# Optimization experiments

Hardware: AMD Instinct MI355X
Metric: run time of the kernel (lower is better)

Reference implementation:

```python
import jax, jax.numpy as jnp
import numpy as np

N, D, S, E, EL, ITERS = 250_000, 128, 6, 500_000, 50_000, 4


def setup_inputs() -> dict:
    key = jax.random.key(0)
    ks = jax.random.split(key, 16)
    s = 1.0 / np.sqrt(D)  # keep activations O(1)
    return {
        'feat':   jax.random.normal(ks[0], (N, D), jnp.float32),
        'pre_u':  jax.random.randint(ks[1], (S, E), 0, N, jnp.int32),
        'pre_v':  jax.random.randint(ks[2], (S, E), 0, N, jnp.int32),
        'suc_u':  jax.random.randint(ks[3], (S, E), 0, N, jnp.int32),
        'suc_v':  jax.random.randint(ks[4], (S, E), 0, N, jnp.int32),
        'left_u': jax.random.randint(ks[5], (EL,), 0, N, jnp.int32),
        'left_v': jax.random.randint(ks[6], (EL,), 0, N, jnp.int32),
        'right_u': jax.random.randint(ks[7], (EL,), 0, N, jnp.int32),
        'right_v': jax.random.randint(ks[8], (EL,), 0, N, jnp.int32),
        'W_ctr':   jax.random.normal(ks[9],  (ITERS, D, D), jnp.float32) * s,
        'W_pre':   jax.random.normal(ks[10], (ITERS, S, D, D), jnp.float32) * s,
        'W_suc':   jax.random.normal(ks[11], (ITERS, S, D, D), jnp.float32) * s,
        'W_left':  jax.random.normal(ks[12], (ITERS, D, D), jnp.float32) * s,
        'W_right': jax.random.normal(ks[13], (ITERS, D, D), jnp.float32) * s,
        'gn1_w': jnp.ones((ITERS, D), jnp.float32),
        'gn1_b': jnp.zeros((ITERS, D), jnp.float32),
        'W_ctr2':  jax.random.normal(ks[14], (ITERS, D, D), jnp.float32) * s,
        'gn2_w': jnp.ones((ITERS, D), jnp.float32),
        'gn2_b': jnp.zeros((ITERS, D), jnp.float32),
    }


def _gn(x, w, b, eps=1e-5):
    # torch GroupNorm(1, D) on a [N, D] input: per-row normalization over channels
    mu = jnp.mean(x, -1, keepdims=True)
    var = jnp.mean((x - mu) ** 2, -1, keepdims=True)
    return (x - mu) * jax.lax.rsqrt(var + eps) * w + b


def reference(feat, pre_u, pre_v, suc_u, suc_v, left_u, left_v, right_u, right_v,
              W_ctr, W_pre, W_suc, W_left, W_right, gn1_w, gn1_b,
              W_ctr2, gn2_w, gn2_b):
    res = feat
    for i in range(ITERS):  # 4 fusion iterations, structurally distinct weights
        temp = feat @ W_ctr[i].T  # nn.Linear(bias=False): x @ W.T
        for k in range(S):  # 6 dilation scales, pre and suc edges
            temp = temp.at[pre_u[k]].add(feat[pre_v[k]] @ W_pre[i, k].T)
            temp = temp.at[suc_u[k]].add(feat[suc_v[k]] @ W_suc[i, k].T)
        temp = temp.at[left_u].add(feat[left_v] @ W_left[i].T)
        temp = temp.at[right_u].add(feat[right_v] @ W_right[i].T)
        h = jax.nn.relu(_gn(temp, gn1_w[i], gn1_b[i]))           # fuse['norm'] + relu
        h = _gn(h @ W_ctr2[i].T, gn2_w[i], gn2_b[i])             # fuse['ctr2']: Linear+GN, no act
        feat = jax.nn.relu(h + res)                              # residual + relu
        res = feat
    return feat
```

## Files before the change

kernel.cpp:

```cpp
#include <hip/hip_runtime.h>


#define NN 250000
#define DD 128
#define EE 500000
#define ELE 50000
#define NITER 4
#define NL 14
#define M14 (NL*NN)
#define TOTE (12*EE + 2*ELE)
#define KBIG (15*DD)
#define BK 64
#define TILES_TOTAL ((NN + 127)/128)
#define NBKT TILES_TOTAL
#define BCAP 4096
#define LK (128*NL)
#define NBLK_BUCKET 256
#define EPB ((TOTE + NBLK_BUCKET - 1)/NBLK_BUCKET)

typedef unsigned short u16;
typedef __attribute__((ext_vector_type(4))) float f32x4;
typedef __attribute__((ext_vector_type(8))) __bf16 bf16x8;

static __device__ __forceinline__ unsigned f2bf(float f) {
  unsigned u = __float_as_uint(f);
  return (u + 0x7fffu + ((u >> 16) & 1u)) >> 16;
}
static __device__ __forceinline__ float bflo(unsigned w){ return __uint_as_float(w << 16); }
static __device__ __forceinline__ float bfhi(unsigned w){ return __uint_as_float(w & 0xffff0000u); }

static __device__ __forceinline__ void gload16(const u16* g, u16* l) {
  __builtin_amdgcn_global_load_lds(
      (const __attribute__((address_space(1))) void*)g,
      (__attribute__((address_space(3))) void*)l, 16, 0, 0);
}

static __device__ __forceinline__ int edge_u(int idx,
    const int* __restrict__ pu, const int* __restrict__ su,
    const int* __restrict__ lu, const int* __restrict__ ru) {
  if (idx < 12*EE) {
    int l = idx / EE; int e = idx - l*EE;
    return (l < 6) ? pu[l*EE + e] : su[(l-6)*EE + e];
  }
  int r = idx - 12*EE;
  return (r < ELE) ? lu[r] : ru[r - ELE];
}

static __device__ __forceinline__ void edge_luv(int idx,
    const int* __restrict__ pu, const int* __restrict__ pv,
    const int* __restrict__ su, const int* __restrict__ sv,
    const int* __restrict__ lu, const int* __restrict__ lv,
    const int* __restrict__ ru, const int* __restrict__ rv,
    int& l, int& u, int& v) {
  if (idx < 12*EE) {
    l = idx / EE; int e = idx - l*EE;
    if (l < 6) { u = pu[l*EE+e]; v = pv[l*EE+e]; }
    else       { u = su[(l-6)*EE+e]; v = sv[(l-6)*EE+e]; }
  } else {
    int r = idx - 12*EE;
    if (r < ELE) { l = 12; u = lu[r]; v = lv[r]; }
    else         { l = 13; u = ru[r-ELE]; v = rv[r-ELE]; }
  }
}

__global__ __launch_bounds__(1024) void k_bucket(
    const int* __restrict__ pu, const int* __restrict__ pv,
    const int* __restrict__ su, const int* __restrict__ sv,
    const int* __restrict__ lu, const int* __restrict__ lv,
    const int* __restrict__ ru, const int* __restrict__ rv,
    int* __restrict__ bcur, unsigned* __restrict__ bstage) {
  __shared__ int cnt[NBKT];
  __shared__ int cur[NBKT];
  int t = threadIdx.x;
  for (int i=t; i<NBKT; i+=1024) cnt[i] = 0;
  __syncthreads();
  int e0 = blockIdx.x * EPB;
  int e1 = e0 + EPB; if (e1 > TOTE) e1 = TOTE;
  for (int idx = e0 + t; idx < e1; idx += 1024) {
    int u = edge_u(idx, pu, su, lu, ru);
    atomicAdd(&cnt[u >> 7], 1);
  }
  __syncthreads();
  for (int i=t; i<NBKT; i+=1024) {
    int c = cnt[i];
    cur[i] = c ? atomicAdd(&bcur[i], c) : 0;
  }
  __syncthreads();
  for (int idx = e0 + t; idx < e1; idx += 1024) {
    int l, u, v;
    edge_luv(idx, pu, pv, su, sv, lu, lv, ru, rv, l, u, v);
    int b = u >> 7;
    unsigned rec = ((unsigned)((u & 127)*NL + l) << 18) | (unsigned)v;
    int pos = atomicAdd(&cur[b], 1);
    if (pos < BCAP) bstage[(size_t)b*BCAP + pos] = rec;
  }
}

__global__ void k_bscan(const int* __restrict__ bcur, int* __restrict__ bbase,
                        int* __restrict__ rowptr) {
  __shared__ int wsum[4];
  int t = threadIdx.x, lane = t & 63, w = t >> 6;
  int v[8]; int s = 0;
  #pragma unroll
  for (int j=0;j<8;j++){
    int idx = t*8 + j;
    int x = 0;
    if (idx < NBKT) { x = bcur[idx]; if (x > BCAP) x = BCAP; }
    v[j] = s; s += x;
  }
  int ps = s;
  for (int d=1; d<64; d<<=1) { int o = __shfl_up(ps, d); if (lane >= d) ps += o; }
  if (lane == 63) wsum[w] = ps;
  __syncthreads();
  int woff = 0;
  for (int j=0;j<w;j++) woff += wsum[j];
  int excl = woff + ps - s;
  #pragma unroll
  for (int j=0;j<8;j++){
    int idx = t*8 + j;
    if (idx < NBKT) bbase[idx] = excl + v[j];
  }
  if (t == 255) rowptr[M14] = excl + s;
}

__global__ __launch_bounds__(256) void k_place(const unsigned* __restrict__ bstage,
    const int* __restrict__ bcur, const int* __restrict__ bbase,
    int* __restrict__ rowptr, int* __restrict__ edge_v) {
  __shared__ int lh[LK];
  __shared__ int lex[LK];
  __shared__ int wsum[4];
  int b = blockIdx.x, t = threadIdx.x;
  int lane = t & 63, w = t >> 6;
  int cnt = bcur[b]; if (cnt > BCAP) cnt = BCAP;
  int base = bbase[b];
  const unsigned* rec = bstage + (size_t)b*BCAP;
  for (int i=t; i<LK; i+=256) lh[i] = 0;
  __syncthreads();
  for (int e=t; e<cnt; e+=256) atomicAdd(&lh[rec[e]>>18], 1);
  __syncthreads();
  int s = 0;
  int my[7];
  #pragma unroll
  for (int j=0;j<7;j++){ my[j] = s; s += lh[t*7+j]; }
  int ps = s;
  for (int d=1; d<64; d<<=1) { int o = __shfl_up(ps, d); if (lane >= d) ps += o; }
  if (lane == 63) wsum[w] = ps;
  __syncthreads();
  int woff = 0;
  for (int j=0;j<w;j++) woff += wsum[j];
  int excl = woff + ps - s;
  #pragma unroll
  for (int j=0;j<7;j++) lex[t*7+j] = excl + my[j];
  __syncthreads();
  for (int i=t; i<LK; i+=256) rowptr[(size_t)b*LK + i] = base + lex[i];
  for (int i=t; i<LK; i+=256) lh[i] = lex[i];
  __syncthreads();
  for (int e=t; e<cnt; e+=256) {
    unsigned r = rec[e];
    int pos = atomicAdd(&lh[r>>18], 1);
    edge_v[base + pos] = (int)(r & 0x3FFFFu);
  }
}

__global__ void k_f2bf(const float* __restrict__ in, unsigned* __restrict__ out) {
  int i = blockIdx.x*256 + threadIdx.x;
  float2 v = ((const float2*)in)[i];
  out[i] = f2bf(v.x) | (f2bf(v.y) << 16);
}

__global__ void k_bw(const float* __restrict__ Wc, const float* __restrict__ Wp,
                     const float* __restrict__ Ws, const float* __restrict__ Wl,
                     const float* __restrict__ Wr, const float* __restrict__ Wc2,
                     int it, u16* __restrict__ wcat, u16* __restrict__ wc2) {
  int i = blockIdx.x*256 + threadIdx.x;
  if (i < 128*KBIG) {
    int r = i / KBIG, K = i - r*KBIG;
    int s = K >> 7, c = K & 127;
    float val;
    if (s == 0)       val = Wc[(it*128 + r)*128 + c];
    else if (s <= 6)  val = Wp[((it*6 + (s-1))*128 + r)*128 + c];
    else if (s <= 12) val = Ws[((it*6 + (s-7))*128 + r)*128 + c];
    else if (s == 13) val = Wl[(it*128 + r)*128 + c];
    else              val = Wr[(it*128 + r)*128 + c];
    wcat[i] = (u16)f2bf(val);
  } else {
    int j = i - 128*KBIG;
    wc2[j] = (u16)f2bf(Wc2[it*16384 + j]);
  }
}

__global__ __launch_bounds__(256) void k_agg(const unsigned* __restrict__ featbf,
    const int* __restrict__ rowptr, const int* __restrict__ edge_v,
    unsigned* __restrict__ X, int chunk_base) {
  int wid = threadIdx.x >> 6, lane = threadIdx.x & 63;
  int nl = blockIdx.x*4 + wid;
  int node = chunk_base + nl;
  size_t xb = (size_t)nl * (14*64);
  if (node >= NN) {
    #pragma unroll
    for (int s=0;s<14;s++) X[xb + s*64 + lane] = 0;
    return;
  }
  int rp = 0;
  if (lane < 15) rp = rowptr[node*NL + lane];
  int st0 = __shfl(rp, 0);
  int cnt = __shfl(rp, 14) - st0;
  float ax = 0.f, ay = 0.f;
  int s = 0;
  int nextb = __shfl(rp, 1);
  int vv = 0;
  for (int base = 0; base < cnt; base += 8) {
    if ((base & 63) == 0) vv = edge_v[st0 + base + lane];
    unsigned wrow[8];
    int m = cnt - base; if (m > 8) m = 8;
    #pragma unroll
    for (int q=0;q<8;q++)
      if (q < m) {
        int v = __shfl(vv, (base & 63) + q);
        wrow[q] = featbf[(size_t)v*64 + lane];
      }
    for (int q=0;q<m;q++) {
      int e = st0 + base + q;
      while (e == nextb && s < 14) {
        X[xb + s*64 + lane] = f2bf(ax) | (f2bf(ay) << 16);
        ax = 0.f; ay = 0.f; s++;
        int ni = s + 1; if (ni > 14) ni = 14;
        nextb = __shfl(rp, ni);
      }
      ax += bflo(wrow[q]); ay += bfhi(wrow[q]);
    }
  }
  while (s < 14) {
    X[xb + s*64 + lane] = f2bf(ax) | (f2bf(ay) << 16);
    ax = 0.f; ay = 0.f; s++;
  }
}

__global__ __launch_bounds__(256) void gemm_big(
    const u16* __restrict__ Xc, const u16* __restrict__ fbf,
    const u16* __restrict__ B, unsigned* __restrict__ hbf,
    const float* __restrict__ gw, const float* __restrict__ gb, int row0_abs) {
  __shared__ u16 smem[2*128*BK];
  u16* As = smem; u16* Bs = smem + 128*BK;
  int tid = threadIdx.x, wid = tid >> 6, lane = tid & 63;
  int wm = wid >> 1, wn = wid & 1;
  int tile_row = blockIdx.x * 128;
  f32x4 acc[4][4] = {};
  int srow = lane >> 3, scol = (lane & 7) * 8;
  for (int k0 = 0; k0 < KBIG; k0 += BK) {
    __syncthreads();
    if (k0 < DD) {
      #pragma unroll
      for (int j=0;j<4;j++) {
        int seg = wid + j*4; int r = seg*8 + srow;
        int arow = row0_abs + tile_row + r; if (arow > NN-1) arow = NN-1;
        gload16(fbf + (size_t)arow*DD + (k0 + scol), &As[seg*512]);
        gload16(B + (size_t)r*KBIG + (k0 + scol), &Bs[seg*512]);
      }
    } else {
      #pragma unroll
      for (int j=0;j<4;j++) {
        int seg = wid + j*4; int r = seg*8 + srow;
        gload16(Xc + (size_t)(tile_row + r)*(14*128) + (k0 - DD + scol), &As[seg*512]);
        gload16(B + (size_t)r*KBIG + (k0 + scol), &Bs[seg*512]);
      }
    }
    __syncthreads();
    #pragma unroll
    for (int kk=0; kk<2; kk++) {
      bf16x8 af[4], bfr[4];
      #pragma unroll
      for (int mt=0; mt<4; mt++)
        af[mt] = *(const bf16x8*)&As[(wm*64 + mt*16 + (lane&15))*BK + kk*32 + ((lane>>4)*8)];
      #pragma unroll
      for (int nt=0; nt<4; nt++)
        bfr[nt] = *(const bf16x8*)&Bs[(wn*64 + nt*16 + (lane&15))*BK + kk*32 + ((lane>>4)*8)];
      #pragma unroll
      for (int mt=0; mt<4; mt++)
        #pragma unroll
        for (int nt=0; nt<4; nt++)
          acc[mt][nt] = __builtin_amdgcn_mfma_f32_16x16x32_bf16(af[mt], bfr[nt], acc[mt][nt], 0, 0, 0);
    }
  }
  float* Cs = (float*)smem;
  float2 wv = ((const float2*)gw)[lane];
  float2 bv = ((const float2*)gb)[lane];
  #pragma unroll
  for (int ph=0; ph<2; ph++) {
    __syncthreads();
    if (wm == ph) {
      #pragma unroll
      for (int mt=0;mt<4;mt++)
        #pragma unroll
        for (int nt=0;nt<4;nt++)
          #pragma unroll
          for (int r=0;r<4;r++)
            Cs[(size_t)(mt*16 + ((lane>>4)<<2) + r)*128 + wn*64 + nt*16 + (lane&15)] = acc[mt][nt][r];
    }
    __syncthreads();
    for (int rr=0; rr<16; rr++) {
      int lrow = wid*16 + rr;
      int grow = row0_abs + tile_row + ph*64 + lrow;
      float2 x = ((float2*)(Cs + lrow*128))[lane];
      float s = x.x + x.y, sq = x.x*x.x + x.y*x.y;
      #pragma unroll
      for (int d=1; d<64; d<<=1) { s += __shfl_xor(s,d); sq += __shfl_xor(sq,d); }
      float mu = s*(1.f/DD), var = sq*(1.f/DD) - mu*mu;
      float rs = rsqrtf(var + 1e-5f);
      if (grow < NN) {
        float y0 = fmaxf(fmaf((x.x-mu)*rs, wv.x, bv.x), 0.f);
        float y1 = fmaxf(fmaf((x.y-mu)*rs, wv.y, bv.y), 0.f);
        hbf[(size_t)grow*64 + lane] = f2bf(y0) | (f2bf(y1) << 16);
      }
    }
  }
}

__global__ __launch_bounds__(256) void gemm_sm(
    const u16* __restrict__ A, const u16* __restrict__ B,
    const float* __restrict__ res, float* __restrict__ out32,
    unsigned* __restrict__ featbf,
    const float* __restrict__ gw, const float* __restrict__ gb) {
  __shared__ u16 smem[2*128*BK];
  u16* As = smem; u16* Bs = smem + 128*BK;
  int tid = threadIdx.x, wid = tid >> 6, lane = tid & 63;
  int wm = wid >> 1, wn = wid & 1;
  int tile_row = blockIdx.x * 128;
  f32x4 acc[4][4] = {};
  int srow = lane >> 3, scol = (lane & 7) * 8;
  for (int k0 = 0; k0 < DD; k0 += BK) {
    __syncthreads();
    #pragma unroll
    for (int j=0;j<4;j++) {
      int seg = wid + j*4; int r = seg*8 + srow;
      gload16(A + (size_t)(tile_row + r)*DD + (k0 + scol), &As[seg*512]);
      gload16(B + (size_t)r*DD + (k0 + scol), &Bs[seg*512]);
    }
    __syncthreads();
    #pragma unroll
    for (int kk=0; kk<2; kk++) {
      bf16x8 af[4], bfr[4];
      #pragma unroll
      for (int mt=0; mt<4; mt++)
        af[mt] = *(const bf16x8*)&As[(wm*64 + mt*16 + (lane&15))*BK + kk*32 + ((lane>>4)*8)];
      #pragma unroll
      for (int nt=0; nt<4; nt++)
        bfr[nt] = *(const bf16x8*)&Bs[(wn*64 + nt*16 + (lane&15))*BK + kk*32 + ((lane>>4)*8)];
      #pragma unroll
      for (int mt=0; mt<4; mt++)
        #pragma unroll
        for (int nt=0; nt<4; nt++)
          acc[mt][nt] = __builtin_amdgcn_mfma_f32_16x16x32_bf16(af[mt], bfr[nt], acc[mt][nt], 0, 0, 0);
    }
  }
  float* Cs = (float*)smem;
  float2 wv = ((const float2*)gw)[lane];
  float2 bv = ((const float2*)gb)[lane];
  #pragma unroll
  for (int ph=0; ph<2; ph++) {
    __syncthreads();
    if (wm == ph) {
      #pragma unroll
      for (int mt=0;mt<4;mt++)
        #pragma unroll
        for (int nt=0;nt<4;nt++)
          #pragma unroll
          for (int r=0;r<4;r++)
            Cs[(size_t)(mt*16 + ((lane>>4)<<2) + r)*128 + wn*64 + nt*16 + (lane&15)] = acc[mt][nt][r];
    }
    __syncthreads();
    for (int rr=0; rr<16; rr++) {
      int lrow = wid*16 + rr;
      int grow = tile_row + ph*64 + lrow;
      float2 x = ((float2*)(Cs + lrow*128))[lane];
      float s = x.x + x.y, sq = x.x*x.x + x.y*x.y;
      #pragma unroll
      for (int d=1; d<64; d<<=1) { s += __shfl_xor(s,d); sq += __shfl_xor(sq,d); }
      float mu = s*(1.f/DD), var = sq*(1.f/DD) - mu*mu;
      float rs = rsqrtf(var + 1e-5f);
      if (grow < NN) {
        float2 rv = ((const float2*)(res + (size_t)grow*DD))[lane];
        float o0 = fmaxf(fmaf((x.x-mu)*rs, wv.x, bv.x) + rv.x, 0.f);
        float o1 = fmaxf(fmaf((x.y-mu)*rs, wv.y, bv.y) + rv.y, 0.f);
        ((float2*)(out32 + (size_t)grow*DD))[lane] = make_float2(o0, o1);
        featbf[(size_t)grow*64 + lane] = f2bf(o0) | (f2bf(o1) << 16);
      }
    }
  }
}

extern "C" void kernel_launch(void* const* d_in, const int* in_sizes, int n_in,
                              void* d_out, int out_size, void* d_ws, size_t ws_size,
                              hipStream_t stream) {
  const float* feat_in = (const float*)d_in[0];
  const int* pre_u  = (const int*)d_in[1];
  const int* pre_v  = (const int*)d_in[2];
  const int* suc_u  = (const int*)d_in[3];
  const int* suc_v  = (const int*)d_in[4];
  const int* left_u = (const int*)d_in[5];
  const int* left_v = (const int*)d_in[6];
  const int* right_u= (const int*)d_in[7];
  const int* right_v= (const int*)d_in[8];
  const float* W_ctr  = (const float*)d_in[9];
  const float* W_pre  = (const float*)d_in[10];
  const float* W_suc  = (const float*)d_in[11];
  const float* W_left = (const float*)d_in[12];
  const float* W_right= (const float*)d_in[13];
  const float* gn1w   = (const float*)d_in[14];
  const float* gn1b   = (const float*)d_in[15];
  const float* W_ctr2 = (const float*)d_in[16];
  const float* gn2w   = (const float*)d_in[17];
  const float* gn2b   = (const float*)d_in[18];

  char* ws = (char*)d_ws;
  size_t off = 0;
  auto alloc = [&](size_t bytes) -> char* {
    char* p = ws + off; off += (bytes + 255) & ~(size_t)255; return p;
  };
  float*    feat32 = (float*)   alloc((size_t)NN*DD*4);
  unsigned* featbf = (unsigned*)alloc((size_t)NN*64*4);
  unsigned* hbf    = (unsigned*)alloc((size_t)TILES_TOTAL*128*64*4);
  u16*      wcat   = (u16*)     alloc((size_t)128*KBIG*2);
  u16*      wc2    = (u16*)     alloc((size_t)128*128*2);
  int*      rowptr = (int*)     alloc(((size_t)NBKT*LK + 1)*4);
  int*      edge_v = (int*)     alloc((size_t)(TOTE + 64)*4);
  unsigned* bstage = (unsigned*)alloc((size_t)NBKT*BCAP*4);
  int*      bcur   = (int*)     alloc((size_t)NBKT*4);
  int*      bbase  = (int*)     alloc((size_t)NBKT*4);

  size_t tile_bytes = (size_t)128*(14*128)*2;
  size_t avail = (ws_size > off + 65536) ? (ws_size - off - 65536) : 0;
  int chunk_tiles = (int)(avail / tile_bytes);
  if (chunk_tiles > 256) chunk_tiles = 256;
  if (chunk_tiles < 8) chunk_tiles = 8;
  unsigned* Xc = (unsigned*)alloc((size_t)chunk_tiles * tile_bytes);
  int nchunk = (TILES_TOTAL + chunk_tiles - 1) / chunk_tiles;
  (void)in_sizes; (void)n_in; (void)out_size;

  hipMemsetAsync(bcur, 0, (size_t)NBKT*4, stream);
  k_bucket<<<NBLK_BUCKET, 1024, 0, stream>>>(pre_u, pre_v, suc_u, suc_v,
                                             left_u, left_v, right_u, right_v,
                                             bcur, bstage);
  k_bscan<<<1, 256, 0, stream>>>(bcur, bbase, rowptr);
  k_place<<<NBKT, 256, 0, stream>>>(bstage, bcur, bbase, rowptr, edge_v);

  k_f2bf<<<NN*64/256, 256, 0, stream>>>(feat_in, featbf);

  for (int it = 0; it < NITER; it++) {
    k_bw<<<1024, 256, 0, stream>>>(W_ctr, W_pre, W_suc, W_left, W_right, W_ctr2, it, wcat, wc2);
    for (int c = 0; c < nchunk; c++) {
      int tile0 = c*chunk_tiles;
      int tiles = (TILES_TOTAL - tile0 < chunk_tiles) ? (TILES_TOTAL - tile0) : chunk_tiles;
      int base  = tile0*128;
      k_agg<<<tiles*32, 256, 0, stream>>>(featbf, rowptr, edge_v, Xc, base);
      gemm_big<<<tiles, 256, 0, stream>>>((const u16*)Xc, (const u16*)featbf, wcat,
                                          hbf, gn1w + it*DD, gn1b + it*DD, base);
    }
    gemm_sm<<<TILES_TOTAL, 256, 0, stream>>>((const u16*)hbf, wc2,
        (it == 0 ? feat_in : feat32),
        (it == NITER-1 ? (float*)d_out : feat32), featbf,
        gn2w + it*DD, gn2b + it*DD);
  }
}
```

Measured before the change: 4.939 ms.

## Fuse ctr2 GEMM and second GroupNorm into the aggregation GEMM epilogue

The separate second-GEMM kernel is merged into the main GEMM: the GN1+ReLU output is kept as bf16 in shared memory and multiplied by W_ctr2 in the same block. GN2, the residual add and the ReLU then run directly on MFMA accumulator registers, with per-row statistics reduced through shuffles and a small shared array. This removes the hbf intermediate and the fp32 feature round trip. The residual now comes from ping-pong bf16 feature buffers, which loses some precision compared with the fp32 residual. Shared-memory tiles also get an XOR swizzle to reduce bank conflicts.

```diff
diff --git a/kernel.cpp b/kernel.cpp
--- a/kernel.cpp
+++ b/kernel.cpp
@@ -236,33 +236,39 @@
   }
 }
 
-__global__ __launch_bounds__(256) void gemm_big(
+__global__ __launch_bounds__(256) void gemm_fused(
     const u16* __restrict__ Xc, const u16* __restrict__ fbf,
-    const u16* __restrict__ B, unsigned* __restrict__ hbf,
-    const float* __restrict__ gw, const float* __restrict__ gb, int row0_abs) {
+    const u16* __restrict__ Bw, const u16* __restrict__ wc2g,
+    unsigned* __restrict__ fout, float* __restrict__ out32, int last,
+    const float* __restrict__ g1w, const float* __restrict__ g1b,
+    const float* __restrict__ g2w, const float* __restrict__ g2b,
+    int row0_abs) {
   __shared__ u16 smem[2*128*BK];
+  __shared__ float stats[2][128][2];
   u16* As = smem; u16* Bs = smem + 128*BK;
   int tid = threadIdx.x, wid = tid >> 6, lane = tid & 63;
   int wm = wid >> 1, wn = wid & 1;
+  int g = lane >> 4, l15 = lane & 15, l7 = lane & 7;
   int tile_row = blockIdx.x * 128;
   f32x4 acc[4][4] = {};
-  int srow = lane >> 3, scol = (lane & 7) * 8;
+  int srow8 = lane >> 3;
+  int scol = ((lane & 7) ^ srow8) * 8;
   for (int k0 = 0; k0 < KBIG; k0 += BK) {
     __syncthreads();
     if (k0 < DD) {
       #pragma unroll
       for (int j=0;j<4;j++) {
-        int seg = wid + j*4; int r = seg*8 + srow;
+        int seg = wid + j*4; int r = seg*8 + srow8;
         int arow = row0_abs + tile_row + r; if (arow > NN-1) arow = NN-1;
         gload16(fbf + (size_t)arow*DD + (k0 + scol), &As[seg*512]);
-        gload16(B + (size_t)r*KBIG + (k0 + scol), &Bs[seg*512]);
+        gload16(Bw + (size_t)r*KBIG + (k0 + scol), &Bs[seg*512]);
       }
     } else {
       #pragma unroll
       for (int j=0;j<4;j++) {
-        int seg = wid + j*4; int r = seg*8 + srow;
+        int seg = wid + j*4; int r = seg*8 + srow8;
         gload16(Xc + (size_t)(tile_row + r)*(14*128) + (k0 - DD + scol), &As[seg*512]);
-        gload16(B + (size_t)r*KBIG + (k0 + scol), &Bs[seg*512]);
+        gload16(Bw + (size_t)r*KBIG + (k0 + scol), &Bs[seg*512]);
       }
     }
     __syncthreads();
@@ -271,10 +277,10 @@
       bf16x8 af[4], bfr[4];
       #pragma unroll
       for (int mt=0; mt<4; mt++)
-        af[mt] = *(const bf16x8*)&As[(wm*64 + mt*16 + (lane&15))*BK + kk*32 + ((lane>>4)*8)];
+        af[mt] = *(const bf16x8*)&As[((wm*64 + mt*16 + l15)*BK + kk*32 + g*8) ^ (l7<<3)];
       #pragma unroll
       for (int nt=0; nt<4; nt++)
-        bfr[nt] = *(const bf16x8*)&Bs[(wn*64 + nt*16 + (lane&15))*BK + kk*32 + ((lane>>4)*8)];
+        bfr[nt] = *(const bf16x8*)&Bs[((wn*64 + nt*16 + l15)*BK + kk*32 + g*8) ^ (l7<<3)];
       #pragma unroll
       for (int mt=0; mt<4; mt++)
         #pragma unroll
@@ -282,111 +288,112 @@
           acc[mt][nt] = __builtin_amdgcn_mfma_f32_16x16x32_bf16(af[mt], bfr[nt], acc[mt][nt], 0, 0, 0);
     }
   }
-  float* Cs = (float*)smem;
-  float2 wv = ((const float2*)gw)[lane];
-  float2 bv = ((const float2*)gb)[lane];
-  #pragma unroll
-  for (int ph=0; ph<2; ph++) {
-    __syncthreads();
-    if (wm == ph) {
-      #pragma unroll
-      for (int mt=0;mt<4;mt++)
-        #pragma unroll
-        for (int nt=0;nt<4;nt++)
-          #pragma unroll
-          for (int r=0;r<4;r++)
-            Cs[(size_t)(mt*16 + ((lane>>4)<<2) + r)*128 + wn*64 + nt*16 + (lane&15)] = acc[mt][nt][r];
-    }
-    __syncthreads();
-    for (int rr=0; rr<16; rr++) {
-      int lrow = wid*16 + rr;
-      int grow = row0_abs + tile_row + ph*64 + lrow;
-      float2 x = ((float2*)(Cs + lrow*128))[lane];
-      float s = x.x + x.y, sq = x.x*x.x + x.y*x.y;
-      #pragma unroll
-      for (int d=1; d<64; d<<=1) { s += __shfl_xor(s,d); sq += __shfl_xor(sq,d); }
-      float mu = s*(1.f/DD), var = sq*(1.f/DD) - mu*mu;
+  __syncthreads();
+
+  #pragma unroll
+  for (int mt=0; mt<4; mt++)
+    #pragma unroll
+    for (int r=0; r<4; r++) {
+      float s = 0.f, q = 0.f;
+      #pragma unroll
+      for (int nt=0; nt<4; nt++) { float v = acc[mt][nt][r]; s += v; q += v*v; }
+      #pragma unroll
+      for (int d=1; d<16; d<<=1) { s += __shfl_xor(s, d); q += __shfl_xor(q, d); }
+      if (l15 == 0) {
+        int R = wm*64 + mt*16 + g*4 + r;
+        stats[wn][R][0] = s; stats[wn][R][1] = q;
+      }
+    }
+  __syncthreads();
+
+  float w1[4], b1[4], w2[4], b2[4];
+  #pragma unroll
+  for (int nt=0; nt<4; nt++) {
+    int C = wn*64 + nt*16 + l15;
+    w1[nt] = g1w[C]; b1[nt] = g1b[C];
+    w2[nt] = g2w[C]; b2[nt] = g2b[C];
+  }
+  #pragma unroll
+  for (int mt=0; mt<4; mt++)
+    #pragma unroll
+    for (int r=0; r<4; r++) {
+      int R = wm*64 + mt*16 + g*4 + r;
+      float ts = stats[0][R][0] + stats[1][R][0];
+      float tq = stats[0][R][1] + stats[1][R][1];
+      float mu = ts*(1.f/DD), var = tq*(1.f/DD) - mu*mu;
       float rs = rsqrtf(var + 1e-5f);
-      if (grow < NN) {
-        float y0 = fmaxf(fmaf((x.x-mu)*rs, wv.x, bv.x), 0.f);
-        float y1 = fmaxf(fmaf((x.y-mu)*rs, wv.y, bv.y), 0.f);
-        hbf[(size_t)grow*64 + lane] = f2bf(y0) | (f2bf(y1) << 16);
-      }
-    }
-  }
-}
-
-__global__ __launch_bounds__(256) void gemm_sm(
-    const u16* __restrict__ A, const u16* __restrict__ B,
-    const float* __restrict__ res, float* __restrict__ out32,
-    unsigned* __restrict__ featbf,
-    const float* __restrict__ gw, const float* __restrict__ gb) {
-  __shared__ u16 smem[2*128*BK];
-  u16* As = smem; u16* Bs = smem + 128*BK;
-  int tid = threadIdx.x, wid = tid >> 6, lane = tid & 63;
-  int wm = wid >> 1, wn = wid & 1;
-  int tile_row = blockIdx.x * 128;
-  f32x4 acc[4][4] = {};
-  int srow = lane >> 3, scol = (lane & 7) * 8;
-  for (int k0 = 0; k0 < DD; k0 += BK) {
-    __syncthreads();
-    #pragma unroll
-    for (int j=0;j<4;j++) {
-      int seg = wid + j*4; int r = seg*8 + srow;
-      gload16(A + (size_t)(tile_row + r)*DD + (k0 + scol), &As[seg*512]);
-      gload16(B + (size_t)r*DD + (k0 + scol), &Bs[seg*512]);
-    }
-    __syncthreads();
-    #pragma unroll
-    for (int kk=0; kk<2; kk++) {
-      bf16x8 af[4], bfr[4];
-      #pragma unroll
-      for (int mt=0; mt<4; mt++)
-        af[mt] = *(const bf16x8*)&As[(wm*64 + mt*16 + (lane&15))*BK + kk*32 + ((lane>>4)*8)];
+      #pragma unroll
+      for (int nt=0; nt<4; nt++) {
+        int C = wn*64 + nt*16 + l15;
+        float y = fmaxf(fmaf((acc[mt][nt][r]-mu)*rs, w1[nt], b1[nt]), 0.f);
+        float p = __shfl_xor(y, 1);
+        if (!(lane & 1)) {
+          unsigned word = f2bf(y) | (f2bf(p) << 16);
+          int idx = (R*128 + (C & ~1)) ^ ((R&7)<<3);
+          *(unsigned*)&smem[idx] = word;
+        }
+      }
+    }
+  __syncthreads();
+
+  f32x4 a2[4][4] = {};
+  #pragma unroll
+  for (int kk2=0; kk2<4; kk2++) {
+    bf16x8 wf[4], hf[4];
+    #pragma unroll
+    for (int nt=0; nt<4; nt++)
+      wf[nt] = *(const bf16x8*)&wc2g[(size_t)(wn*64 + nt*16 + l15)*DD + kk2*32 + g*8];
+    #pragma unroll
+    for (int mt=0; mt<4; mt++)
+      hf[mt] = *(const bf16x8*)&smem[((wm*64 + mt*16 + l15)*DD + kk2*32 + g*8) ^ (l7<<3)];
+    #pragma unroll
+    for (int mt=0; mt<4; mt++)
       #pragma unroll
       for (int nt=0; nt<4; nt++)
-        bfr[nt] = *(const bf16x8*)&Bs[(wn*64 + nt*16 + (lane&15))*BK + kk*32 + ((lane>>4)*8)];
-      #pragma unroll
-      for (int mt=0; mt<4; mt++)
-        #pragma unroll
-        for (int nt=0; nt<4; nt++)
-          acc[mt][nt] = __builtin_amdgcn_mfma_f32_16x16x32_bf16(af[mt], bfr[nt], acc[mt][nt], 0, 0, 0);
-    }
-  }
-  float* Cs = (float*)smem;
-  float2 wv = ((const float2*)gw)[lane];
-  float2 bv = ((const float2*)gb)[lane];
-  #pragma unroll
-  for (int ph=0; ph<2; ph++) {
-    __syncthreads();
-    if (wm == ph) {
-      #pragma unroll
-      for (int mt=0;mt<4;mt++)
-        #pragma unroll
-        for (int nt=0;nt<4;nt++)
-          #pragma unroll
-          for (int r=0;r<4;r++)
-            Cs[(size_t)(mt*16 + ((lane>>4)<<2) + r)*128 + wn*64 + nt*16 + (lane&15)] = acc[mt][nt][r];
-    }
-    __syncthreads();
-    for (int rr=0; rr<16; rr++) {
-      int lrow = wid*16 + rr;
-      int grow = tile_row + ph*64 + lrow;
-      float2 x = ((float2*)(Cs + lrow*128))[lane];
-      float s = x.x + x.y, sq = x.x*x.x + x.y*x.y;
-      #pragma unroll
-      for (int d=1; d<64; d<<=1) { s += __shfl_xor(s,d); sq += __shfl_xor(sq,d); }
-      float mu = s*(1.f/DD), var = sq*(1.f/DD) - mu*mu;
+        a2[mt][nt] = __builtin_amdgcn_mfma_f32_16x16x32_bf16(hf[mt], wf[nt], a2[mt][nt], 0, 0, 0);
+  }
+  __syncthreads();
+
+  #pragma unroll
+  for (int mt=0; mt<4; mt++)
+    #pragma unroll
+    for (int r=0; r<4; r++) {
+      float s = 0.f, q = 0.f;
+      #pragma unroll
+      for (int nt=0; nt<4; nt++) { float v = a2[mt][nt][r]; s += v; q += v*v; }
+      #pragma unroll
+      for (int d=1; d<16; d<<=1) { s += __shfl_xor(s, d); q += __shfl_xor(q, d); }
+      if (l15 == 0) {
+        int R = wm*64 + mt*16 + g*4 + r;
+        stats[wn][R][0] = s; stats[wn][R][1] = q;
+      }
+    }
+  __syncthreads();
+
+  #pragma unroll
+  for (int mt=0; mt<4; mt++)
+    #pragma unroll
+    for (int r=0; r<4; r++) {
+      int R = wm*64 + mt*16 + g*4 + r;
+      int grow = row0_abs + tile_row + R;
+      float ts = stats[0][R][0] + stats[1][R][0];
+      float tq = stats[0][R][1] + stats[1][R][1];
+      float mu = ts*(1.f/DD), var = tq*(1.f/DD) - mu*mu;
       float rs = rsqrtf(var + 1e-5f);
-      if (grow < NN) {
-        float2 rv = ((const float2*)(res + (size_t)grow*DD))[lane];
-        float o0 = fmaxf(fmaf((x.x-mu)*rs, wv.x, bv.x) + rv.x, 0.f);
-        float o1 = fmaxf(fmaf((x.y-mu)*rs, wv.y, bv.y) + rv.y, 0.f);
-        ((float2*)(out32 + (size_t)grow*DD))[lane] = make_float2(o0, o1);
-        featbf[(size_t)grow*64 + lane] = f2bf(o0) | (f2bf(o1) << 16);
-      }
-    }
-  }
+      bool ok = grow < NN;
+      #pragma unroll
+      for (int nt=0; nt<4; nt++) {
+        int C = wn*64 + nt*16 + l15;
+        float yv = fmaf((a2[mt][nt][r]-mu)*rs, w2[nt], b2[nt]);
+        unsigned rw = ok ? ((const unsigned*)fbf)[(size_t)grow*64 + (C>>1)] : 0u;
+        float resv = (lane & 1) ? bfhi(rw) : bflo(rw);
+        float o = fmaxf(yv + resv, 0.f);
+        if (last && ok) out32[(size_t)grow*DD + C] = o;
+        float p = __shfl_xor(o, 1);
+        if (!(lane & 1) && ok)
+          fout[(size_t)grow*64 + (C>>1)] = f2bf(o) | (f2bf(p) << 16);
+      }
+    }
 }
 
 extern "C" void kernel_launch(void* const* d_in, const int* in_sizes, int n_in,
@@ -417,9 +424,8 @@
   auto alloc = [&](size_t bytes) -> char* {
     char* p = ws + off; off += (bytes + 255) & ~(size_t)255; return p;
   };
-  float*    feat32 = (float*)   alloc((size_t)NN*DD*4);
-  unsigned* featbf = (unsigned*)alloc((size_t)NN*64*4);
-  unsigned* hbf    = (unsigned*)alloc((size_t)TILES_TOTAL*128*64*4);
+  unsigned* featA  = (unsigned*)alloc((size_t)NN*64*4);
+  unsigned* featB  = (unsigned*)alloc((size_t)NN*64*4);
   u16*      wcat   = (u16*)     alloc((size_t)128*KBIG*2);
   u16*      wc2    = (u16*)     alloc((size_t)128*128*2);
   int*      rowptr = (int*)     alloc(((size_t)NBKT*LK + 1)*4);
@@ -444,21 +450,22 @@
   k_bscan<<<1, 256, 0, stream>>>(bcur, bbase, rowptr);
   k_place<<<NBKT, 256, 0, stream>>>(bstage, bcur, bbase, rowptr, edge_v);
 
-  k_f2bf<<<NN*64/256, 256, 0, stream>>>(feat_in, featbf);
+  k_f2bf<<<NN*64/256, 256, 0, stream>>>(feat_in, featA);
 
   for (int it = 0; it < NITER; it++) {
+    unsigned* fin  = (it & 1) ? featB : featA;
+    unsigned* fo   = (it & 1) ? featA : featB;
+    int last = (it == NITER-1) ? 1 : 0;
     k_bw<<<1024, 256, 0, stream>>>(W_ctr, W_pre, W_suc, W_left, W_right, W_ctr2, it, wcat, wc2);
     for (int c = 0; c < nchunk; c++) {
       int tile0 = c*chunk_tiles;
       int tiles = (TILES_TOTAL - tile0 < chunk_tiles) ? (TILES_TOTAL - tile0) : chunk_tiles;
       int base  = tile0*128;
-      k_agg<<<tiles*32, 256, 0, stream>>>(featbf, rowptr, edge_v, Xc, base);
-      gemm_big<<<tiles, 256, 0, stream>>>((const u16*)Xc, (const u16*)featbf, wcat,
-                                          hbf, gn1w + it*DD, gn1b + it*DD, base);
-    }
-    gemm_sm<<<TILES_TOTAL, 256, 0, stream>>>((const u16*)hbf, wc2,
-        (it == 0 ? feat_in : feat32),
-        (it == NITER-1 ? (float*)d_out : feat32), featbf,
-        gn2w + it*DD, gn2b + it*DD);
-  }
-}
+      k_agg<<<tiles*32, 256, 0, stream>>>(fin, rowptr, edge_v, Xc, base);
+      gemm_fused<<<tiles, 256, 0, stream>>>((const u16*)Xc, (const u16*)fin, wcat, wc2,
+                                            fo, (float*)d_out, last,
+                                            gn1w + it*DD, gn1b + it*DD,
+                                            gn2w + it*DD, gn2b + it*DD, base);
+    }
+  }
+}
```

Result: faster. 4.765 ms (-3.5%).
